# Performance work log

Measured on AMD Instinct MI355X. Metric: run time of the kernel, lower is better.

## Reference

```python
import jax, jax.numpy as jnp
import numpy as np

HIDDEN = 256

def setup_inputs() -> dict:
    key = jax.random.key(0)
    ks = jax.random.split(key, 7)
    B, T, L = 64, 128, 32
    H, OUT, IN = HIDDEN, 128, 2
    s = 1.0 / np.sqrt(H)
    return {
        "x": jax.random.normal(ks[0], (B, T, L, IN), dtype=jnp.float32),
        "W_ih": jax.random.uniform(ks[1], (4 * H, IN), jnp.float32, -s, s),
        "W_hh": jax.random.uniform(ks[2], (4 * H, H), jnp.float32, -s, s),
        "b_ih": jax.random.uniform(ks[3], (4 * H,), jnp.float32, -s, s),
        "b_hh": jax.random.uniform(ks[4], (4 * H,), jnp.float32, -s, s),
        "fc_w": jax.random.uniform(ks[5], (128, H), jnp.float32, -s, s),
        "fc_b": jax.random.uniform(ks[6], (128,), jnp.float32, -s, s),
    }

def _lstm_scan(xs, W_ih, W_hh, b_ih, b_hh):
    # xs: [L, N, in]; returns hs: [L, N, H]
    N = xs.shape[1]
    H = W_hh.shape[1]
    h0 = jnp.zeros((N, H), dtype=xs.dtype)
    c0 = jnp.zeros((N, H), dtype=xs.dtype)
    # precompute input projections for all steps: [L, N, 4H]
    x_proj = jnp.einsum('lni,gi->lng', xs, W_ih) + b_ih + b_hh

    def step(carry, xp):
        h, c = carry
        gates = xp + h @ W_hh.T  # [N, 4H]
        i, f, g, o = jnp.split(gates, 4, axis=-1)  # PyTorch gate order i,f,g,o
        c_new = jax.nn.sigmoid(f) * c + jax.nn.sigmoid(i) * jnp.tanh(g)
        h_new = jax.nn.sigmoid(o) * jnp.tanh(c_new)
        return (h_new, c_new), h_new

    _, hs = jax.lax.scan(step, (h0, c0), x_proj)
    return hs

def reference(x, W_ih, W_hh, b_ih, b_hh, fc_w, fc_b):
    B, T, L, IN = x.shape
    xs = x.reshape(B * T, L, IN).transpose(1, 0, 2)  # [L, N, IN], N = B*T
    hs = _lstm_scan(xs, W_ih, W_hh, b_ih, b_hh)      # [L, N, H]
    out = jnp.einsum('lnh,oh->lno', hs, fc_w) + fc_b  # [L, N, OUT]
    out = out.transpose(1, 0, 2).reshape(B, T, L, -1)
    return out
```

## Files before the change

kernel.cpp:

```cpp
#include <hip/hip_runtime.h>

typedef _Float16 f16;
typedef _Float16 f16x8 __attribute__((ext_vector_type(8)));
typedef float f32x4 __attribute__((ext_vector_type(4)));

#define N_TOT   8192
#define L_STEPS 32
#define H_DIM   256
#define G4      1024
#define OUT_DIM 128
#define BN      32
#define NBLK    256
#define THREADS 512

#define WPACK_OFF  0
#define FCPACK_OFF 524288
#define BSUM_OFF   589824

__global__ __launch_bounds__(256) void prep_kernel(
    const float* __restrict__ W_hh, const float* __restrict__ fc_w,
    const float* __restrict__ b_ih, const float* __restrict__ b_hh,
    f16* __restrict__ Wpack, f16* __restrict__ fcpack, float* __restrict__ bsum)
{
    int p = blockIdx.x * blockDim.x + threadIdx.x;
    if (p < 262144) {
        int e = p & 7, lane = (p >> 3) & 63, T = (p >> 9) & 63, kb = p >> 15;
        int g = 16 * T + (lane & 15);
        int k = 32 * kb + 8 * (lane >> 4) + e;
        Wpack[p] = (f16)W_hh[g * 256 + k];
    } else if (p < 262144 + 32768) {
        int p2 = p - 262144;
        int e = p2 & 7, lane = (p2 >> 3) & 63, ot = (p2 >> 9) & 7, kb = p2 >> 12;
        int o = 16 * ot + (lane & 15);
        int k = 32 * kb + 8 * (lane >> 4) + e;
        fcpack[p2] = (f16)fc_w[o * 256 + k];
    } else if (p < 262144 + 32768 + 1024) {
        int g = p - 262144 - 32768;
        bsum[g] = b_ih[g] + b_hh[g];
    }
}

__device__ __forceinline__ float sigmoid_(float x) {
    return 1.0f / (1.0f + __expf(-x));
}
__device__ __forceinline__ float tanh_(float x) {
    float t = __expf(-2.0f * x);
    return (1.0f - t) / (1.0f + t);
}

__device__ __forceinline__ void lds_barrier() {
    asm volatile("s_waitcnt lgkmcnt(0)" ::: "memory");
    __builtin_amdgcn_s_barrier();
    asm volatile("" ::: "memory");
}

__global__ __launch_bounds__(THREADS, 2) void lstm_kernel(
    const float* __restrict__ x, const float* __restrict__ W_ih,
    const f16* __restrict__ Wpack, const float* __restrict__ bsum,
    const f16* __restrict__ fcpack, const float* __restrict__ fc_b,
    float* __restrict__ out)
{
    __shared__ __align__(16) f16 hp[2][8192];
    __shared__ __align__(16) float obuf[BN * OUT_DIM];

    const int tid  = threadIdx.x;
    const int wave = tid >> 6;
    const int lane = tid & 63;
    const int l15  = lane & 15;
    const int lq   = lane >> 4;
    const int n0   = blockIdx.x * BN;
    const int kb0  = (blockIdx.x >> 3) & 7;

    f16x8 fcw[8];
#pragma unroll
    for (int kb = 0; kb < 8; ++kb)
        fcw[kb] = *(const f16x8*)&fcpack[((kb * 8 + wave) * 64 + lane) * 8];

    for (int i = tid; i < 8192; i += THREADS) hp[0][i] = (f16)0.0f;

    float wih0[2][4], wih1[2][4], bsv[2][4];
#pragma unroll
    for (int ti = 0; ti < 2; ++ti)
#pragma unroll
        for (int q = 0; q < 4; ++q) {
            int g = 256 * q + 16 * (wave + 8 * ti) + l15;
            wih0[ti][q] = W_ih[g * 2 + 0];
            wih1[ti][q] = W_ih[g * 2 + 1];
            bsv[ti][q]  = bsum[g];
        }
    const float fcbv = fc_b[16 * wave + l15];

    float c[2][2][4];
#pragma unroll
    for (int ti = 0; ti < 2; ++ti)
#pragma unroll
        for (int mt = 0; mt < 2; ++mt)
#pragma unroll
            for (int r = 0; r < 4; ++r) c[ti][mt][r] = 0.0f;

    unsigned long long wb_u =
        (unsigned long long)(uintptr_t)(Wpack + wave * 512 + lane * 8);

    f16x8 wbuf[2][2][4];
    {
        const f16* wb = (const f16*)(uintptr_t)wb_u;
#pragma unroll
        for (int ti = 0; ti < 2; ++ti)
#pragma unroll
            for (int q = 0; q < 4; ++q)
                wbuf[0][ti][q] = *(const f16x8*)&wb[kb0 * 32768 + q * 8192 + ti * 4096];
    }

    float2 xc[2][4];
#pragma unroll
    for (int mt = 0; mt < 2; ++mt)
#pragma unroll
        for (int r = 0; r < 4; ++r) {
            int n = n0 + 16 * mt + 4 * lq + r;
            xc[mt][r] = *(const float2*)&x[(n * L_STEPS + 0) * 2];
        }

    __syncthreads();

    int buf = 0;
#pragma unroll 1
    for (int l = 0; l < L_STEPS; ++l) {
        asm volatile("" : "+v"(wb_u));
        const f16* wb = (const f16*)(uintptr_t)wb_u;

        f32x4 acc[2][2][4];
#pragma unroll
        for (int mt = 0; mt < 2; ++mt)
#pragma unroll
            for (int r = 0; r < 4; ++r) {
#pragma unroll
                for (int ti = 0; ti < 2; ++ti)
#pragma unroll
                    for (int q = 0; q < 4; ++q)
                        acc[ti][mt][q][r] = bsv[ti][q] + xc[mt][r].x * wih0[ti][q]
                                                       + xc[mt][r].y * wih1[ti][q];
            }

        float2 xn[2][4];
        if (l + 1 < L_STEPS) {
#pragma unroll
            for (int mt = 0; mt < 2; ++mt)
#pragma unroll
                for (int r = 0; r < 4; ++r) {
                    int n = n0 + 16 * mt + 4 * lq + r;
                    xn[mt][r] = *(const float2*)&x[(n * L_STEPS + l + 1) * 2];
                }
        }

#pragma unroll
        for (int p = 0; p < 8; ++p) {
            int kb_c = (p + kb0) & 7;
            int kb_n = (p + 1 + kb0) & 7;
#pragma unroll
            for (int ti = 0; ti < 2; ++ti)
#pragma unroll
                for (int q = 0; q < 4; ++q)
                    wbuf[(p + 1) & 1][ti][q] =
                        *(const f16x8*)&wb[kb_n * 32768 + q * 8192 + ti * 4096];

            f16x8 a0 = *(const f16x8*)&hp[buf][((kb_c * 2 + 0) * 64 + lane) * 8];
            f16x8 a1 = *(const f16x8*)&hp[buf][((kb_c * 2 + 1) * 64 + lane) * 8];
#pragma unroll
            for (int ti = 0; ti < 2; ++ti)
#pragma unroll
                for (int q = 0; q < 4; ++q) {
                    acc[ti][0][q] = __builtin_amdgcn_mfma_f32_16x16x32_f16(
                        a0, wbuf[p & 1][ti][q], acc[ti][0][q], 0, 0, 0);
                    acc[ti][1][q] = __builtin_amdgcn_mfma_f32_16x16x32_f16(
                        a1, wbuf[p & 1][ti][q], acc[ti][1][q], 0, 0, 0);
                }
        }

#pragma unroll
        for (int ti = 0; ti < 2; ++ti) {
            int j   = 16 * (wave + 8 * ti) + l15;
            int kbj = j >> 5, qk = (j >> 3) & 3, e = j & 7;
#pragma unroll
            for (int mt = 0; mt < 2; ++mt)
#pragma unroll
                for (int r = 0; r < 4; ++r) {
                    float gi = acc[ti][mt][0][r];
                    float gf = acc[ti][mt][1][r];
                    float gg = acc[ti][mt][2][r];
                    float go = acc[ti][mt][3][r];
                    float cn = sigmoid_(gf) * c[ti][mt][r] + sigmoid_(gi) * tanh_(gg);
                    c[ti][mt][r] = cn;
                    float hv = sigmoid_(go) * tanh_(cn);
                    int laneA = (4 * lq + r) | (qk << 4);
                    hp[buf ^ 1][((kbj * 2 + mt) * 64 + laneA) * 8 + e] = (f16)hv;
                }
        }
        lds_barrier();

        f32x4 facc0 = {fcbv, fcbv, fcbv, fcbv};
        f32x4 facc1 = facc0;
#pragma unroll
        for (int kb = 0; kb < 8; ++kb) {
            f16x8 a0 = *(const f16x8*)&hp[buf ^ 1][((kb * 2 + 0) * 64 + lane) * 8];
            f16x8 a1 = *(const f16x8*)&hp[buf ^ 1][((kb * 2 + 1) * 64 + lane) * 8];
            facc0 = __builtin_amdgcn_mfma_f32_16x16x32_f16(a0, fcw[kb], facc0, 0, 0, 0);
            facc1 = __builtin_amdgcn_mfma_f32_16x16x32_f16(a1, fcw[kb], facc1, 0, 0, 0);
        }
        const int o = 16 * wave + l15;
#pragma unroll
        for (int r = 0; r < 4; ++r) {
            obuf[(4 * lq + r) * OUT_DIM + o]        = facc0[r];
            obuf[(16 + 4 * lq + r) * OUT_DIM + o]   = facc1[r];
        }
        lds_barrier();

        {
            const int row = tid >> 4;
            const int gl  = ((n0 + row) * L_STEPS + l) * OUT_DIM;
#pragma unroll
            for (int half = 0; half < 2; ++half) {
                int col = (tid & 15) * 4 + half * 64;
                f32x4 v = *(const f32x4*)&obuf[row * OUT_DIM + col];
                *(f32x4*)&out[gl + col] = v;
            }
        }

#pragma unroll
        for (int mt = 0; mt < 2; ++mt)
#pragma unroll
            for (int r = 0; r < 4; ++r) xc[mt][r] = xn[mt][r];
        buf ^= 1;
    }
}

extern "C" void kernel_launch(void* const* d_in, const int* in_sizes, int n_in,
                              void* d_out, int out_size, void* d_ws, size_t ws_size,
                              hipStream_t stream) {
    const float* x    = (const float*)d_in[0];
    const float* W_ih = (const float*)d_in[1];
    const float* W_hh = (const float*)d_in[2];
    const float* b_ih = (const float*)d_in[3];
    const float* b_hh = (const float*)d_in[4];
    const float* fc_w = (const float*)d_in[5];
    const float* fc_b = (const float*)d_in[6];
    float* out = (float*)d_out;

    char* ws = (char*)d_ws;
    f16*   Wpack  = (f16*)(ws + WPACK_OFF);
    f16*   fcpack = (f16*)(ws + FCPACK_OFF);
    float* bsum   = (float*)(ws + BSUM_OFF);

    const int prep_elems = 262144 + 32768 + 1024;
    prep_kernel<<<(prep_elems + 255) / 256, 256, 0, stream>>>(
        W_hh, fc_w, b_ih, b_hh, Wpack, fcpack, bsum);

    lstm_kernel<<<NBLK, THREADS, 0, stream>>>(
        x, W_ih, Wpack, bsum, fcpack, fc_b, out);
}
```

Baseline: 466.1 us.

## Fuse FC projection into next step's recurrent MFMA loop and triple-buffer weights

Computes the output projection for step l-1 inside step l's recurrent MFMA loop, reusing the same h fragments from LDS. This removes the second FC pass, the obuf staging and one barrier per step, and writes the results directly to global memory with scalar stores. The W_hh prefetch becomes a 3-deep rotating buffer issued after each MFMA group, and pointers are cast to global address space. In exchange it uses more registers, which could spill or lower occupancy, and the direct output stores are less coalesced than before.

```diff
diff --git a/kernel.cpp b/kernel.cpp
--- a/kernel.cpp
+++ b/kernel.cpp
@@ -4,10 +4,12 @@
 typedef _Float16 f16x8 __attribute__((ext_vector_type(8)));
 typedef float f32x4 __attribute__((ext_vector_type(4)));
 
+typedef __attribute__((address_space(1))) const f16 gf16;
+typedef __attribute__((address_space(1))) const f16x8 gf16x8;
+
 #define N_TOT   8192
 #define L_STEPS 32
 #define H_DIM   256
-#define G4      1024
 #define OUT_DIM 128
 #define BN      32
 #define NBLK    256
@@ -61,7 +63,6 @@
     float* __restrict__ out)
 {
     __shared__ __align__(16) f16 hp[2][8192];
-    __shared__ __align__(16) float obuf[BN * OUT_DIM];
 
     const int tid  = threadIdx.x;
     const int wave = tid >> 6;
@@ -73,8 +74,10 @@
 
     f16x8 fcw[8];
 #pragma unroll
-    for (int kb = 0; kb < 8; ++kb)
-        fcw[kb] = *(const f16x8*)&fcpack[((kb * 8 + wave) * 64 + lane) * 8];
+    for (int p = 0; p < 8; ++p) {
+        int kb = (p + kb0) & 7;
+        fcw[p] = *(const f16x8*)&fcpack[((kb * 8 + wave) * 64 + lane) * 8];
+    }
 
     for (int i = tid; i < 8192; i += THREADS) hp[0][i] = (f16)0.0f;
 
@@ -89,6 +92,7 @@
             bsv[ti][q]  = bsum[g];
         }
     const float fcbv = fc_b[16 * wave + l15];
+    const int   ocol = 16 * wave + l15;
 
     float c[2][2][4];
 #pragma unroll
@@ -101,14 +105,19 @@
     unsigned long long wb_u =
         (unsigned long long)(uintptr_t)(Wpack + wave * 512 + lane * 8);
 
-    f16x8 wbuf[2][2][4];
+    f16x8 wbuf[3][2][4];
     {
-        const f16* wb = (const f16*)(uintptr_t)wb_u;
-#pragma unroll
-        for (int ti = 0; ti < 2; ++ti)
-#pragma unroll
-            for (int q = 0; q < 4; ++q)
-                wbuf[0][ti][q] = *(const f16x8*)&wb[kb0 * 32768 + q * 8192 + ti * 4096];
+        gf16* wb = (gf16*)(uintptr_t)wb_u;
+#pragma unroll
+        for (int s = 0; s < 3; ++s) {
+            int kb = (kb0 + s) & 7;
+#pragma unroll
+            for (int ti = 0; ti < 2; ++ti)
+#pragma unroll
+                for (int q = 0; q < 4; ++q)
+                    wbuf[s][ti][q] =
+                        *(const gf16x8*)&wb[kb * 32768 + q * 8192 + ti * 4096];
+        }
     }
 
     float2 xc[2][4];
@@ -126,7 +135,7 @@
 #pragma unroll 1
     for (int l = 0; l < L_STEPS; ++l) {
         asm volatile("" : "+v"(wb_u));
-        const f16* wb = (const f16*)(uintptr_t)wb_u;
+        gf16* wb = (gf16*)(uintptr_t)wb_u;
 
         f32x4 acc[2][2][4];
 #pragma unroll
@@ -141,6 +150,9 @@
                                                        + xc[mt][r].y * wih1[ti][q];
             }
 
+        f32x4 facc0 = {fcbv, fcbv, fcbv, fcbv};
+        f32x4 facc1 = facc0;
+
         float2 xn[2][4];
         if (l + 1 < L_STEPS) {
 #pragma unroll
@@ -154,14 +166,8 @@
 
 #pragma unroll
         for (int p = 0; p < 8; ++p) {
-            int kb_c = (p + kb0) & 7;
-            int kb_n = (p + 1 + kb0) & 7;
-#pragma unroll
-            for (int ti = 0; ti < 2; ++ti)
-#pragma unroll
-                for (int q = 0; q < 4; ++q)
-                    wbuf[(p + 1) & 1][ti][q] =
-                        *(const f16x8*)&wb[kb_n * 32768 + q * 8192 + ti * 4096];
+            const int s    = p % 3;
+            const int kb_c = (p + kb0) & 7;
 
             f16x8 a0 = *(const f16x8*)&hp[buf][((kb_c * 2 + 0) * 64 + lane) * 8];
             f16x8 a1 = *(const f16x8*)&hp[buf][((kb_c * 2 + 1) * 64 + lane) * 8];
@@ -170,10 +176,29 @@
 #pragma unroll
                 for (int q = 0; q < 4; ++q) {
                     acc[ti][0][q] = __builtin_amdgcn_mfma_f32_16x16x32_f16(
-                        a0, wbuf[p & 1][ti][q], acc[ti][0][q], 0, 0, 0);
+                        a0, wbuf[s][ti][q], acc[ti][0][q], 0, 0, 0);
                     acc[ti][1][q] = __builtin_amdgcn_mfma_f32_16x16x32_f16(
-                        a1, wbuf[p & 1][ti][q], acc[ti][1][q], 0, 0, 0);
+                        a1, wbuf[s][ti][q], acc[ti][1][q], 0, 0, 0);
                 }
+            facc0 = __builtin_amdgcn_mfma_f32_16x16x32_f16(a0, fcw[p], facc0, 0, 0, 0);
+            facc1 = __builtin_amdgcn_mfma_f32_16x16x32_f16(a1, fcw[p], facc1, 0, 0, 0);
+
+            const int pn   = (p <= 4) ? (p + 3) : (p == 5 ? 2 : (p == 6 ? 0 : 1));
+            const int kb_n = (pn + kb0) & 7;
+#pragma unroll
+            for (int ti = 0; ti < 2; ++ti)
+#pragma unroll
+                for (int q = 0; q < 4; ++q)
+                    wbuf[s][ti][q] =
+                        *(const gf16x8*)&wb[kb_n * 32768 + q * 8192 + ti * 4096];
+        }
+
+        if (l > 0) {
+#pragma unroll
+            for (int r = 0; r < 4; ++r) {
+                out[((n0 + 4 * lq + r) * L_STEPS + (l - 1)) * OUT_DIM + ocol]      = facc0[r];
+                out[((n0 + 16 + 4 * lq + r) * L_STEPS + (l - 1)) * OUT_DIM + ocol] = facc1[r];
+            }
         }
 
 #pragma unroll
@@ -197,39 +222,29 @@
         }
         lds_barrier();
 
-        f32x4 facc0 = {fcbv, fcbv, fcbv, fcbv};
-        f32x4 facc1 = facc0;
-#pragma unroll
-        for (int kb = 0; kb < 8; ++kb) {
-            f16x8 a0 = *(const f16x8*)&hp[buf ^ 1][((kb * 2 + 0) * 64 + lane) * 8];
-            f16x8 a1 = *(const f16x8*)&hp[buf ^ 1][((kb * 2 + 1) * 64 + lane) * 8];
-            facc0 = __builtin_amdgcn_mfma_f32_16x16x32_f16(a0, fcw[kb], facc0, 0, 0, 0);
-            facc1 = __builtin_amdgcn_mfma_f32_16x16x32_f16(a1, fcw[kb], facc1, 0, 0, 0);
-        }
-        const int o = 16 * wave + l15;
-#pragma unroll
-        for (int r = 0; r < 4; ++r) {
-            obuf[(4 * lq + r) * OUT_DIM + o]        = facc0[r];
-            obuf[(16 + 4 * lq + r) * OUT_DIM + o]   = facc1[r];
-        }
-        lds_barrier();
-
-        {
-            const int row = tid >> 4;
-            const int gl  = ((n0 + row) * L_STEPS + l) * OUT_DIM;
-#pragma unroll
-            for (int half = 0; half < 2; ++half) {
-                int col = (tid & 15) * 4 + half * 64;
-                f32x4 v = *(const f32x4*)&obuf[row * OUT_DIM + col];
-                *(f32x4*)&out[gl + col] = v;
-            }
-        }
-
 #pragma unroll
         for (int mt = 0; mt < 2; ++mt)
 #pragma unroll
             for (int r = 0; r < 4; ++r) xc[mt][r] = xn[mt][r];
         buf ^= 1;
+    }
+
+    {
+        f32x4 e0 = {fcbv, fcbv, fcbv, fcbv};
+        f32x4 e1 = e0;
+#pragma unroll
+        for (int p = 0; p < 8; ++p) {
+            const int kb_c = (p + kb0) & 7;
+            f16x8 a0 = *(const f16x8*)&hp[buf][((kb_c * 2 + 0) * 64 + lane) * 8];
+            f16x8 a1 = *(const f16x8*)&hp[buf][((kb_c * 2 + 1) * 64 + lane) * 8];
+            e0 = __builtin_amdgcn_mfma_f32_16x16x32_f16(a0, fcw[p], e0, 0, 0, 0);
+            e1 = __builtin_amdgcn_mfma_f32_16x16x32_f16(a1, fcw[p], e1, 0, 0, 0);
+        }
+#pragma unroll
+        for (int r = 0; r < 4; ++r) {
+            out[((n0 + 4 * lq + r) * L_STEPS + 31) * OUT_DIM + ocol]      = e0[r];
+            out[((n0 + 16 + 4 * lq + r) * L_STEPS + 31) * OUT_DIM + ocol] = e1[r];
+        }
     }
 }
 
```

Result: slower. 756.7 us (+62.3%).
